# Performance work log

Measured on AMD Instinct MI355X. Metric: run time of the kernel, lower is better.

## Reference

```python
import jax, jax.numpy as jnp
import numpy as np

N = 50000      # n_nodes
E = 800000     # edges (before self-loops)
IN = 128       # in_dim
HID = 32       # hidden_dim (per-head out channels)
HEADS = 4
EMB = 128      # embed_dim
LAYERS = 3
NEG_SLOPE = 0.2  # PyG GATv2 default leaky_relu slope


def _layer_norm(x, g, b):
    mu = jnp.mean(x, axis=-1, keepdims=True)
    var = jnp.var(x, axis=-1, keepdims=True)
    return g * (x - mu) / jnp.sqrt(var + 1e-5) + b


def _gatv2(h, src, dst, n, Wl, bl, Wr, br, att, bias):
    # GATv2Conv (PyG semantics, share_weights=False, concat=True).
    H, C = att.shape
    xl = (h @ Wl + bl).reshape(n, H, C)   # target (i) transform
    xr = (h @ Wr + br).reshape(n, H, C)   # source (j) transform
    x_i = xl[dst]                          # [Etot, H, C] gather
    x_j = xr[src]
    e = jax.nn.leaky_relu(x_i + x_j, NEG_SLOPE)
    logit = jnp.einsum('ehc,hc->eh', e, att)          # [Etot, H]
    # segment softmax over destination node (every node has a self-loop)
    m = jax.ops.segment_max(logit, dst, num_segments=n)
    ex = jnp.exp(logit - m[dst])
    den = jax.ops.segment_sum(ex, dst, num_segments=n)
    alpha = ex / (den[dst] + 1e-16)
    out = jax.ops.segment_sum(alpha[..., None] * x_j, dst, num_segments=n)
    return out.reshape(n, H * C) + bias


def setup_inputs() -> dict:
    key = jax.random.key(0)
    ks = iter(jax.random.split(key, 64))
    d = {}
    d['x'] = jax.random.normal(next(ks), (N, IN), jnp.float32)
    d['edge_index'] = jax.random.randint(next(ks), (2, E), 0, N, dtype=jnp.int64)

    def w(shape, fan):
        return jax.random.normal(next(ks), shape, jnp.float32) / np.float32(np.sqrt(fan))

    HC = HID * HEADS
    d['W_in'] = w((IN, HID), IN); d['b_in'] = jnp.zeros((HID,), jnp.float32)
    for i in range(LAYERS):
        ic = HID if i == 0 else HC
        d[f'Wl{i}'] = w((ic, HC), ic); d[f'bl{i}'] = jnp.zeros((HC,), jnp.float32)
        d[f'Wr{i}'] = w((ic, HC), ic); d[f'br{i}'] = jnp.zeros((HC,), jnp.float32)
        d[f'att{i}'] = w((HEADS, HID), HID)
        d[f'bo{i}'] = jnp.zeros((HC,), jnp.float32)
        d[f'g{i}'] = jnp.ones((HC,), jnp.float32)
        d[f'be{i}'] = jnp.zeros((HC,), jnp.float32)
    d['W_out'] = w((HC, EMB), HC); d['b_out'] = jnp.zeros((EMB,), jnp.float32)
    return d


def reference(x, edge_index, W_in, b_in,
              Wl0, bl0, Wr0, br0, att0, bo0, g0, be0,
              Wl1, bl1, Wr1, br1, att1, bo1, g1, be1,
              Wl2, bl2, Wr2, br2, att2, bo2, g2, be2,
              W_out, b_out):
    n = x.shape[0]
    loops = jnp.arange(n, dtype=edge_index.dtype)  # add_self_loops=True
    src = jnp.concatenate([edge_index[0], loops])
    dst = jnp.concatenate([edge_index[1], loops])

    h = jax.nn.gelu(x @ W_in + b_in, approximate=False)
    layers = [(Wl0, bl0, Wr0, br0, att0, bo0, g0, be0),
              (Wl1, bl1, Wr1, br1, att1, bo1, g1, be1),
              (Wl2, bl2, Wr2, br2, att2, bo2, g2, be2)]
    for (Wl, bl, Wr, br, att, bo, g, be) in layers:
        h_new = jax.nn.gelu(_layer_norm(_gatv2(h, src, dst, n, Wl, bl, Wr, br, att, bo), g, be), approximate=False)
        h = h + h_new if h.shape == h_new.shape else h_new  # dropout = identity (eval)
    out = h @ W_out + b_out
    norm = jnp.maximum(jnp.linalg.norm(out, axis=-1, keepdims=True), 1e-12)
    return out / norm
```

## Files before the change

### kernel.cpp

```cpp
#include <hip/hip_runtime.h>
#include <hip/hip_bf16.h>
#include <math.h>

#define N_NODES 50000
#define N_EDGES 800000
#define IN_DIM  128
#define HC_DIM  128
#define HID_C   32
#define SCAN_NB 196
#define LOG2E   1.4426950408889634f

typedef __attribute__((ext_vector_type(8))) short short8;
typedef __attribute__((ext_vector_type(4))) float f32x4;
typedef _Float16 hf8 __attribute__((ext_vector_type(8)));
typedef unsigned int uint4v __attribute__((ext_vector_type(4)));

__device__ __forceinline__ float gelu_f(float x){
    return 0.5f*x*(1.0f + erff(x*0.7071067811865475f));
}

__device__ __forceinline__ void split2(float f, short& h, short& l){
    __hip_bfloat16 bh = __float2bfloat16(f);
    float r = f - __bfloat162float(bh);
    __hip_bfloat16 blo = __float2bfloat16(r);
    h = *reinterpret_cast<short*>(&bh);
    l = *reinterpret_cast<short*>(&blo);
}
__device__ __forceinline__ unsigned short f2h(float f){
    _Float16 h = (_Float16)f;
    return __builtin_bit_cast(unsigned short, h);
}
__device__ __forceinline__ float bf2f(unsigned short u){
    return __uint_as_float(((unsigned)u)<<16);
}

__global__ __launch_bounds__(256) void k_count(const int* __restrict__ dst, int* __restrict__ cnt,
                                               int* __restrict__ rank){
    int b = blockIdx.x*1024 + threadIdx.x;
    #pragma unroll
    for(int i=0;i<4;i++){
        int e = b + i*256;
        if(e < N_EDGES) rank[e] = atomicAdd(&cnt[dst[e]], 1);
    }
}

__global__ __launch_bounds__(256) void k_scan1(const int* __restrict__ cnt, int* __restrict__ rowptr,
                                               int* __restrict__ part){
    __shared__ int sh[256];
    int t=threadIdx.x; int i=blockIdx.x*256+t;
    int v = (i<N_NODES)? cnt[i] : 0;
    sh[t]=v; __syncthreads();
    for(int off=1; off<256; off<<=1){
        int y = (t>=off)? sh[t-off] : 0;
        __syncthreads();
        sh[t] += y;
        __syncthreads();
    }
    if(i<N_NODES) rowptr[i] = sh[t]-v;
    if(t==255) part[blockIdx.x] = sh[255];
}

__global__ __launch_bounds__(256) void k_scan2(int* __restrict__ part){
    __shared__ int sh[256];
    int t=threadIdx.x;
    int v = (t<SCAN_NB)? part[t] : 0;
    sh[t]=v; __syncthreads();
    for(int off=1; off<256; off<<=1){
        int y=(t>=off)? sh[t-off]:0;
        __syncthreads();
        sh[t]+=y;
        __syncthreads();
    }
    if(t<SCAN_NB) part[t] = sh[t]-v;
}

__global__ __launch_bounds__(256) void k_scan3(int* __restrict__ rowptr, const int* __restrict__ part){
    int t=threadIdx.x; int i=blockIdx.x*256+t;
    if(i<N_NODES) rowptr[i] += part[blockIdx.x];
    if(i==0) rowptr[N_NODES]=N_EDGES;
}

__global__ __launch_bounds__(256) void k_fill(const int* __restrict__ src, const int* __restrict__ dst,
                                              const int* __restrict__ rowptr, const int* __restrict__ rank,
                                              int* __restrict__ col){
    int b = blockIdx.x*1024 + threadIdx.x;
    #pragma unroll
    for(int i=0;i<4;i++){
        int e = b + i*256;
        if(e < N_EDGES) col[rowptr[dst[e]] + rank[e]] = src[e];
    }
}

__global__ __launch_bounds__(256) void k_splitW(const float* __restrict__ W0, const float* __restrict__ W1,
                                                const float* __restrict__ W2, const float* __restrict__ W3,
                                                const float* __restrict__ W4, const float* __restrict__ W5,
                                                const float* __restrict__ W6, short* __restrict__ WT){
    int bx = blockIdx.x;
    int m, kc;
    if(bx < 2){ m = bx; kc = 0; }
    else { m = 2 + (bx-2)/4; kc = (bx-2)&3; }
    const float* src; int K; size_t off;
    switch(m){
        case 0: src=W0; K=32;  off=0;      break;
        case 1: src=W1; K=32;  off=8192;   break;
        case 2: src=W2; K=128; off=16384;  break;
        case 3: src=W3; K=128; off=49152;  break;
        case 4: src=W4; K=128; off=81920;  break;
        case 5: src=W5; K=128; off=114688; break;
        default:src=W6; K=128; off=147456; break;
    }
    short* hi = WT + off;
    short* lo = hi + (size_t)K*HC_DIM;
    #pragma unroll
    for(int i=0;i<16;i++){
        int idx = threadIdx.x + i*256;
        int k = kc*32 + (idx>>7);
        int n = idx & 127;
        float f = src[(size_t)k*HC_DIM + n];
        short h,l; split2(f,h,l);
        hi[(size_t)n*K + k] = h;
        lo[(size_t)n*K + k] = l;
    }
}

__global__ __launch_bounds__(256) void k_gemm_in(const float* __restrict__ x, const float* __restrict__ W,
                                                 const float* __restrict__ b,
                                                 short* __restrict__ hhi, short* __restrict__ hlo){
    int id = blockIdx.x*256+threadIdx.x;
    int r = id>>5, c = id&31;
    const float4* x4 = (const float4*)(x + (size_t)r*IN_DIM);
    float acc=0.f;
    #pragma unroll 8
    for(int k=0;k<IN_DIM/4;k++){
        float4 xv = x4[k];
        acc = fmaf(xv.x, W[(4*k  )*HID_C+c], acc);
        acc = fmaf(xv.y, W[(4*k+1)*HID_C+c], acc);
        acc = fmaf(xv.z, W[(4*k+2)*HID_C+c], acc);
        acc = fmaf(xv.w, W[(4*k+3)*HID_C+c], acc);
    }
    float v = gelu_f(acc + b[c]);
    short hh,ll; split2(v,hh,ll);
    hhi[(size_t)r*HID_C+c] = hh;
    hlo[(size_t)r*HID_C+c] = ll;
}

template<int K, bool PAIR, bool NORM>
__global__ __launch_bounds__(256) void k_mm(const short* __restrict__ Ahi, const short* __restrict__ Alo,
                                            const short* __restrict__ WTl, const float* __restrict__ bl,
                                            const short* __restrict__ WTr, const float* __restrict__ br,
                                            float* __restrict__ XLf, unsigned short* __restrict__ XLh,
                                            unsigned short* __restrict__ XR16){
    constexpr int LDS_K = 40;
    constexpr int NCH = K / 32;
    __shared__ short As_hi[64*LDS_K], As_lo[64*LDS_K];
    __shared__ short Bh0[128*LDS_K], Bl0[128*LDS_K];
    __shared__ short Bh1[PAIR?128*LDS_K:1], Bl1[PAIR?128*LDS_K:1];
    __shared__ float ssq[NORM?256:1];

    int t = threadIdx.x;
    int lane = t & 63, wave = t >> 6;
    int quad = lane >> 4, ml = lane & 15;
    int rbase = blockIdx.x * 64;

    const short* WTl_lo = WTl + (size_t)K*HC_DIM;
    const short* WTr_lo = PAIR ? (WTr + (size_t)K*HC_DIM) : nullptr;

    f32x4 accL[4][2], accR[4][2];
    #pragma unroll
    for(int i=0;i<4;i++)
        #pragma unroll
        for(int j=0;j<2;j++){ accL[i][j]=(f32x4){0,0,0,0}; accR[i][j]=(f32x4){0,0,0,0}; }

    int r = t >> 2, seg = t & 3;
    int gr = rbase + r; if(gr >= N_NODES) gr = N_NODES-1;

    for(int c=0; c<NCH; c++){
        if(c) __syncthreads();
        size_t ka = (size_t)gr*K + c*32 + seg*8;
        *(short8*)(As_hi + r*LDS_K + seg*8) = *(const short8*)(Ahi + ka);
        *(short8*)(As_lo + r*LDS_K + seg*8) = *(const short8*)(Alo + ka);
        #pragma unroll
        for(int u=0; u<2; u++){
            int uu = t + u*256;
            int n = uu >> 2, sg = uu & 3;
            size_t kw = (size_t)n*K + c*32 + sg*8;
            *(short8*)(Bh0 + n*LDS_K + sg*8) = *(const short8*)(WTl + kw);
            *(short8*)(Bl0 + n*LDS_K + sg*8) = *(const short8*)(WTl_lo + kw);
            if(PAIR){
                *(short8*)(Bh1 + n*LDS_K + sg*8) = *(const short8*)(WTr + kw);
                *(short8*)(Bl1 + n*LDS_K + sg*8) = *(const short8*)(WTr_lo + kw);
            }
        }
        __syncthreads();

        int k0 = quad*8;
        short8 ah[4], al[4];
        #pragma unroll
        for(int i=0;i<4;i++){
            ah[i] = *(const short8*)(As_hi + (16*i + ml)*LDS_K + k0);
            al[i] = *(const short8*)(As_lo + (16*i + ml)*LDS_K + k0);
        }
        #pragma unroll
        for(int j=0;j<2;j++){
            int nrow = j*64 + wave*16 + ml;
            short8 bh = *(const short8*)(Bh0 + nrow*LDS_K + k0);
            short8 blo = *(const short8*)(Bl0 + nrow*LDS_K + k0);
            #pragma unroll
            for(int i=0;i<4;i++){
                accL[i][j] = __builtin_amdgcn_mfma_f32_16x16x32_bf16(ah[i], bh,  accL[i][j], 0,0,0);
                accL[i][j] = __builtin_amdgcn_mfma_f32_16x16x32_bf16(ah[i], blo, accL[i][j], 0,0,0);
                accL[i][j] = __builtin_amdgcn_mfma_f32_16x16x32_bf16(al[i], bh,  accL[i][j], 0,0,0);
            }
            if(PAIR){
                short8 ch = *(const short8*)(Bh1 + nrow*LDS_K + k0);
                short8 cl = *(const short8*)(Bl1 + nrow*LDS_K + k0);
                #pragma unroll
                for(int i=0;i<4;i++){
                    accR[i][j] = __builtin_amdgcn_mfma_f32_16x16x32_bf16(ah[i], ch, accR[i][j], 0,0,0);
                    accR[i][j] = __builtin_amdgcn_mfma_f32_16x16x32_bf16(ah[i], cl, accR[i][j], 0,0,0);
                    accR[i][j] = __builtin_amdgcn_mfma_f32_16x16x32_bf16(al[i], ch, accR[i][j], 0,0,0);
                }
            }
        }
    }

    int col0 = wave*16 + ml, col1 = 64 + wave*16 + ml;
    float bL0 = bl[col0], bL1 = bl[col1];

    if(NORM){
        #pragma unroll
        for(int i=0;i<4;i++){
            #pragma unroll
            for(int rr=0;rr<4;rr++){
                float v0 = accL[i][0][rr] + bL0;
                float v1 = accL[i][1][rr] + bL1;
                float p = v0*v0 + v1*v1;
                p += __shfl_xor(p,1); p += __shfl_xor(p,2);
                p += __shfl_xor(p,4); p += __shfl_xor(p,8);
                if(ml==0) ssq[wave*64 + 16*i + quad*4 + rr] = p;
            }
        }
        __syncthreads();
        #pragma unroll
        for(int i=0;i<4;i++){
            #pragma unroll
            for(int rr=0;rr<4;rr++){
                int row = 16*i + quad*4 + rr;
                int grr = rbase + row;
                if(grr < N_NODES){
                    float tot = ssq[row] + ssq[64+row] + ssq[128+row] + ssq[192+row];
                    float inv = 1.0f / fmaxf(sqrtf(tot), 1e-12f);
                    XLf[(size_t)grr*HC_DIM + col0] = (accL[i][0][rr] + bL0) * inv;
                    XLf[(size_t)grr*HC_DIM + col1] = (accL[i][1][rr] + bL1) * inv;
                }
            }
        }
    } else {
        float bR0 = PAIR ? br[col0] : 0.f, bR1 = PAIR ? br[col1] : 0.f;
        #pragma unroll
        for(int i=0;i<4;i++){
            #pragma unroll
            for(int rr=0;rr<4;rr++){
                int grr = rbase + 16*i + quad*4 + rr;
                if(grr < N_NODES){
                    XLh[(size_t)grr*HC_DIM + col0] = f2h(accL[i][0][rr] + bL0);
                    XLh[(size_t)grr*HC_DIM + col1] = f2h(accL[i][1][rr] + bL1);
                    if(PAIR){
                        XR16[(size_t)grr*HC_DIM + col0] = f2h(accR[i][0][rr] + bR0);
                        XR16[(size_t)grr*HC_DIM + col1] = f2h(accR[i][1][rr] + bR1);
                    }
                }
            }
        }
    }
}

__global__ __launch_bounds__(256) void k_node(const unsigned short* __restrict__ XLH, const unsigned short* __restrict__ XR,
    const int* __restrict__ rowptr, const int* __restrict__ colidx,
    const float* __restrict__ att, const float* __restrict__ bo,
    const float* __restrict__ gg, const float* __restrict__ be,
    const short* __restrict__ hold_hi, const short* __restrict__ hold_lo,
    short* __restrict__ hi_out, short* __restrict__ lo_out)
{
    int wave=threadIdx.x>>6, lane=threadIdx.x&63;
    int qd = lane >> 4, cl = lane & 15;
    int c8 = cl << 3;
    int ch2 = c8 + (qd<<1);

    float4 aa = *(const float4*)(att + c8);
    float4 abv = *(const float4*)(att + c8 + 4);
    float af[8] = {aa.x,aa.y,aa.z,aa.w,abv.x,abv.y,abv.z,abv.w};
    hf8 av6, av4;
    const float s6 = 0.6f*LOG2E, s4 = 0.4f*LOG2E;
    #pragma unroll
    for(int k=0;k<8;k++){
        av6[k] = (_Float16)(af[k]*s6);
        av4[k] = (_Float16)(af[k]*s4);
    }
    float4 b0 = *(const float4*)(bo + c8);
    float4 b1 = *(const float4*)(bo + c8 + 4);
    float bof[8] = {b0.x,b0.y,b0.z,b0.w,b1.x,b1.y,b1.z,b1.w};
    float2 g2  = *(const float2*)(gg + ch2);
    float2 be2 = *(const float2*)(be + ch2);

    #define H2(v,k) __builtin_shufflevector(v, v, 2*(k), 2*(k)+1)
    #define LOADH(j, xv) { xv = *(const hf8*)((const _Float16*)XR + ((size_t)((unsigned)(j)<<7)) + c8); }
#if defined(__has_builtin) && __has_builtin(__builtin_amdgcn_fdot2)
    #define LOGIT(xv, q) { \
        hf8 u_ = xlh + xv; \
        hf8 a_ = __builtin_bit_cast(hf8, __builtin_bit_cast(uint4v, u_) & 0x7fff7fffu); \
        float qa_ = __builtin_amdgcn_fdot2(H2(u_,0), H2(av6,0), 0.f, false); \
        float qb_ = __builtin_amdgcn_fdot2(H2(a_,0), H2(av4,0), 0.f, false); \
        qa_ = __builtin_amdgcn_fdot2(H2(u_,1), H2(av6,1), qa_, false); \
        qb_ = __builtin_amdgcn_fdot2(H2(a_,1), H2(av4,1), qb_, false); \
        qa_ = __builtin_amdgcn_fdot2(H2(u_,2), H2(av6,2), qa_, false); \
        qb_ = __builtin_amdgcn_fdot2(H2(a_,2), H2(av4,2), qb_, false); \
        qa_ = __builtin_amdgcn_fdot2(H2(u_,3), H2(av6,3), qa_, false); \
        qb_ = __builtin_amdgcn_fdot2(H2(a_,3), H2(av4,3), qb_, false); \
        q = qa_ + qb_; \
        q += __shfl_xor(q,1); q += __shfl_xor(q,2); }
#else
    #define LOGIT(xv, q) { \
        hf8 u_ = xlh + xv; \
        hf8 a_ = __builtin_bit_cast(hf8, __builtin_bit_cast(uint4v, u_) & 0x7fff7fffu); \
        q = 0.f; \
        _Pragma("unroll") \
        for(int k_=0;k_<8;k_++) q = fmaf((float)u_[k_], (float)av6[k_], fmaf((float)a_[k_], (float)av4[k_], q)); \
        q += __shfl_xor(q,1); q += __shfl_xor(q,2); }
#endif
    #define UPDATE4 { \
        float nm = fmaxf(m, fmaxf(fmaxf(q0,q1),fmaxf(q2,q3))); \
        float sc = exp2f(m-nm); \
        float e0=exp2f(q0-nm), e1=exp2f(q1-nm), e2=exp2f(q2-nm), e3=exp2f(q3-nm); \
        ls = fmaf(ls, sc, (e0+e1)+(e2+e3)); \
        _Pragma("unroll") \
        for(int k=0;k<8;k++) \
            acc[k] = fmaf(acc[k], sc, fmaf(e0,(float)x0[k], fmaf(e1,(float)x1[k], fmaf(e2,(float)x2[k], e3*(float)x3[k])))); \
        m = nm; }

    int nstep = gridDim.x << 2;
    for(int node = (blockIdx.x<<2) + wave; node < N_NODES; node += nstep){

        int beg = rowptr[node], end = rowptr[node+1];
        hf8 xlh = *(const hf8*)((const _Float16*)XLH + ((size_t)((unsigned)node<<7)) + c8);
        hf8 xs; LOADH(node, xs)
        float hres0 = 0.f, hres1 = 0.f;
        if(hold_hi){
            short2 hh = *(const short2*)(hold_hi + (size_t)node*HC_DIM + ch2);
            short2 hl = *(const short2*)(hold_lo + (size_t)node*HC_DIM + ch2);
            hres0 = bf2f((unsigned short)hh.x) + bf2f((unsigned short)hl.x);
            hres1 = bf2f((unsigned short)hh.y) + bf2f((unsigned short)hl.y);
        }

        float qs; LOGIT(xs, qs)
        float m, ls, acc[8];
        if(qd==0){
            m = qs; ls = 1.f;
            #pragma unroll
            for(int k=0;k<8;k++) acc[k] = (float)xs[k];
        } else {
            m = -1e30f; ls = 0.f;
            #pragma unroll
            for(int k=0;k<8;k++) acc[k] = 0.f;
        }

        int P = end - beg;
        int nb = P >> 4;
        int base = beg;
        int qoff = qd << 2;
        for(int b=0; b<nb; b++, base += 16){
            int b2 = base + qoff;
            int j0 = colidx[b2], j1 = colidx[b2+1], j2 = colidx[b2+2], j3 = colidx[b2+3];
            hf8 x0,x1,x2,x3;
            LOADH(j0,x0) LOADH(j1,x1) LOADH(j2,x2) LOADH(j3,x3)
            float q0,q1,q2,q3;
            LOGIT(x0,q0) LOGIT(x1,q1) LOGIT(x2,q2) LOGIT(x3,q3)
            UPDATE4
        }
        if(base < end){
            int b2 = base + qoff;
            int j0 = (b2  <end)? colidx[b2]   : node;
            int j1 = (b2+1<end)? colidx[b2+1] : node;
            int j2 = (b2+2<end)? colidx[b2+2] : node;
            int j3 = (b2+3<end)? colidx[b2+3] : node;
            hf8 x0,x1,x2,x3;
            LOADH(j0,x0) LOADH(j1,x1) LOADH(j2,x2) LOADH(j3,x3)
            float q0,q1,q2,q3;
            LOGIT(x0,q0) LOGIT(x1,q1) LOGIT(x2,q2) LOGIT(x3,q3)
            if(b2+1>=end) q1 = -INFINITY;
            if(b2+2>=end) q2 = -INFINITY;
            if(b2+3>=end) q3 = -INFINITY;
            if(b2 < end){
                UPDATE4
            }
        }

        #pragma unroll
        for(int mk=16; mk<=32; mk<<=1){
            float mo  = __shfl_xor(m, mk);
            float lso = __shfl_xor(ls, mk);
            float ao[8];
            #pragma unroll
            for(int k=0;k<8;k++) ao[k] = __shfl_xor(acc[k], mk);
            float nm = fmaxf(m, mo);
            float s0 = exp2f(m-nm), s1 = exp2f(mo-nm);
            ls = ls*s0 + lso*s1;
            #pragma unroll
            for(int k=0;k<8;k++) acc[k] = acc[k]*s0 + ao[k]*s1;
            m = nm;
        }

        float inv = 1.0f/ls;
        float o[8];
        #pragma unroll
        for(int k=0;k<8;k++) o[k] = fmaf(acc[k], inv, bof[k]);
        float s1v = ((o[0]+o[1])+(o[2]+o[3])) + ((o[4]+o[5])+(o[6]+o[7]));
        float s2v = o[0]*o[0];
        #pragma unroll
        for(int k=1;k<8;k++) s2v = fmaf(o[k],o[k],s2v);
        #pragma unroll
        for(int mk=1;mk<16;mk<<=1){ s1v += __shfl_xor(s1v,mk); s2v += __shfl_xor(s2v,mk); }
        float mean = s1v*(1.f/128.f);
        float var  = s2v*(1.f/128.f) - mean*mean;
        float rstd = rsqrtf(var + 1e-5f);

        float oa = (qd&2) ? ((qd&1)? o[6] : o[4]) : ((qd&1)? o[2] : o[0]);
        float ob = (qd&2) ? ((qd&1)? o[7] : o[5]) : ((qd&1)? o[3] : o[1]);
        float r0 = gelu_f(fmaf(g2.x*(oa-mean), rstd, be2.x)) + hres0;
        float r1 = gelu_f(fmaf(g2.y*(ob-mean), rstd, be2.y)) + hres1;
        short h0,l0,h1,l1;
        split2(r0,h0,l0); split2(r1,h1,l1);
        *(short2*)(hi_out + (size_t)node*HC_DIM + ch2) = make_short2(h0,h1);
        *(short2*)(lo_out + (size_t)node*HC_DIM + ch2) = make_short2(l0,l1);
    }
    #undef UPDATE4
    #undef LOGIT
    #undef LOADH
    #undef H2
}

extern "C" void kernel_launch(void* const* d_in, const int* in_sizes, int n_in,
                              void* d_out, int out_size, void* d_ws, size_t ws_size,
                              hipStream_t stream)
{
    const float* x   = (const float*)d_in[0];
    const int*   ei  = (const int*)  d_in[1];
    const float* Win = (const float*)d_in[2];
    const float* bin = (const float*)d_in[3];
    const float *Wl[3], *bl[3], *Wr[3], *br[3], *att[3], *bo[3], *gg[3], *be[3];
    for(int i=0;i<3;i++){
        const int base = 4 + 8*i;
        Wl[i]=(const float*)d_in[base+0]; bl[i]=(const float*)d_in[base+1];
        Wr[i]=(const float*)d_in[base+2]; br[i]=(const float*)d_in[base+3];
        att[i]=(const float*)d_in[base+4]; bo[i]=(const float*)d_in[base+5];
        gg[i]=(const float*)d_in[base+6]; be[i]=(const float*)d_in[base+7];
    }
    const float* Wout=(const float*)d_in[28];
    const float* bout=(const float*)d_in[29];
    float* out = (float*)d_out;

    char* w = (char*)d_ws;
    unsigned short* XLH = (unsigned short*)w; w += (size_t)N_NODES*HC_DIM*2;
    unsigned short* XR16 = (unsigned short*)w; w += (size_t)N_NODES*HC_DIM*2;
    short* hAhi = (short*)w; w += (size_t)N_NODES*HC_DIM*2;
    short* hAlo = (short*)w; w += (size_t)N_NODES*HC_DIM*2;
    short* hBhi = (short*)w; w += (size_t)N_NODES*HC_DIM*2;
    short* hBlo = (short*)w; w += (size_t)N_NODES*HC_DIM*2;
    short* WT   = (short*)w; w += (size_t)180224*2;
    int* rowptr = (int*)w;  w += (size_t)(N_NODES+2)*4;
    int* cursor = (int*)w;  w += (size_t)N_NODES*4;
    int* colidx = (int*)w;  w += (size_t)N_EDGES*4;
    int* rank   = (int*)w;  w += (size_t)N_EDGES*4;
    int* part   = (int*)w;  w += 256*4;

    const int* srcp = ei;
    const int* dstp = ei + N_EDGES;

    const short* WTl0 = WT + 0;      const short* WTr0 = WT + 8192;
    const short* WTl1 = WT + 16384;  const short* WTr1 = WT + 49152;
    const short* WTl2 = WT + 81920;  const short* WTr2 = WT + 114688;
    const short* WTo  = WT + 147456;

    k_splitW<<<22,256,0,stream>>>(Wl[0],Wr[0],Wl[1],Wr[1],Wl[2],Wr[2],Wout, WT);
    hipMemsetAsync(cursor, 0, (size_t)N_NODES*4, stream);
    k_count <<<782,256, 0, stream>>>(dstp, cursor, rank);
    k_scan1 <<<SCAN_NB,256,0,stream>>>(cursor, rowptr, part);
    k_scan2 <<<1,   256, 0, stream>>>(part);
    k_scan3 <<<SCAN_NB,256,0,stream>>>(rowptr, part);
    k_fill  <<<782,256, 0, stream>>>(srcp, dstp, rowptr, rank, colidx);
    k_gemm_in<<<6250,256,0,stream>>>(x, Win, bin, hAhi, hAlo);

    k_mm<32,true,false><<<782,256,0,stream>>>(hAhi, hAlo, WTl0, bl[0], WTr0, br[0],
                                              nullptr, XLH, XR16);
    k_node<<<2048,256,0,stream>>>(XLH,XR16,rowptr,colidx,att[0],bo[0],gg[0],be[0],
                                  (const short*)nullptr, (const short*)nullptr, hBhi, hBlo);

    k_mm<128,true,false><<<782,256,0,stream>>>(hBhi, hBlo, WTl1, bl[1], WTr1, br[1],
                                               nullptr, XLH, XR16);
    k_node<<<2048,256,0,stream>>>(XLH,XR16,rowptr,colidx,att[1],bo[1],gg[1],be[1],
                                  hBhi, hBlo, hAhi, hAlo);

    k_mm<128,true,false><<<782,256,0,stream>>>(hAhi, hAlo, WTl2, bl[2], WTr2, br[2],
                                               nullptr, XLH, XR16);
    k_node<<<2048,256,0,stream>>>(XLH,XR16,rowptr,colidx,att[2],bo[2],gg[2],be[2],
                                  hAhi, hAlo, hBhi, hBlo);

    k_mm<128,false,true><<<782,256,0,stream>>>(hBhi, hBlo, WTo, bout, nullptr, nullptr,
                                               out, nullptr, nullptr);
}
```

Before: 505.2 us.

## Merge preprocessing kernels, fuse scan phases, and launch one wave per node

Weight splitting, the cursor memset and the input GEMM now run as one combined prep kernel. The three-stage scan becomes two passes: a last-block-done atomic performs the partial-sum scan, and the fill kernel applies the offsets while writing a finalized rowptr. The node kernel drops its grid-stride loop and launches one wave per node with 12500 blocks. The goal is fewer kernel launches and less serialization between small kernels. The cost is a threadfence/atomic dependency and more blocks in the node kernel.

After: 518.3 us. 2.6% more time.

```diff
diff --git a/kernel.cpp b/kernel.cpp
--- a/kernel.cpp
+++ b/kernel.cpp
@@ -9,6 +9,9 @@
 #define HID_C   32
 #define SCAN_NB 196
 #define LOG2E   1.4426950408889634f
+#define PREP_SPLITW 22
+#define PREP_MEMSET 49
+#define PREP_GEMM   6250
 
 typedef __attribute__((ext_vector_type(8))) short short8;
 typedef __attribute__((ext_vector_type(4))) float f32x4;
@@ -34,6 +37,69 @@
     return __uint_as_float(((unsigned)u)<<16);
 }
 
+__global__ __launch_bounds__(256) void k_prep(const float* __restrict__ W0, const float* __restrict__ W1,
+                                              const float* __restrict__ W2, const float* __restrict__ W3,
+                                              const float* __restrict__ W4, const float* __restrict__ W5,
+                                              const float* __restrict__ W6, short* __restrict__ WT,
+                                              int* __restrict__ cursor, int* __restrict__ flag,
+                                              const float* __restrict__ x, const float* __restrict__ Win,
+                                              const float* __restrict__ bin,
+                                              short* __restrict__ hhi, short* __restrict__ hlo){
+    int bx = blockIdx.x;
+    if(bx < PREP_SPLITW){
+        int m, kc;
+        if(bx < 2){ m = bx; kc = 0; }
+        else { m = 2 + (bx-2)/4; kc = (bx-2)&3; }
+        const float* src; int K; size_t off;
+        switch(m){
+            case 0: src=W0; K=32;  off=0;      break;
+            case 1: src=W1; K=32;  off=8192;   break;
+            case 2: src=W2; K=128; off=16384;  break;
+            case 3: src=W3; K=128; off=49152;  break;
+            case 4: src=W4; K=128; off=81920;  break;
+            case 5: src=W5; K=128; off=114688; break;
+            default:src=W6; K=128; off=147456; break;
+        }
+        short* hi = WT + off;
+        short* lo = hi + (size_t)K*HC_DIM;
+        #pragma unroll
+        for(int i=0;i<16;i++){
+            int idx = threadIdx.x + i*256;
+            int k = kc*32 + (idx>>7);
+            int n = idx & 127;
+            float f = src[(size_t)k*HC_DIM + n];
+            short h,l; split2(f,h,l);
+            hi[(size_t)n*K + k] = h;
+            lo[(size_t)n*K + k] = l;
+        }
+    } else if(bx < PREP_SPLITW + PREP_MEMSET){
+        int base = (bx - PREP_SPLITW)*1024 + threadIdx.x;
+        #pragma unroll
+        for(int i=0;i<4;i++){
+            int e = base + i*256;
+            if(e < N_NODES) cursor[e] = 0;
+        }
+        if(bx == PREP_SPLITW && threadIdx.x == 0) *flag = 0;
+    } else {
+        int id = (bx - PREP_SPLITW - PREP_MEMSET)*256 + threadIdx.x;
+        int r = id>>5, c = id&31;
+        const float4* x4 = (const float4*)(x + (size_t)r*IN_DIM);
+        float acc=0.f;
+        #pragma unroll 8
+        for(int k=0;k<IN_DIM/4;k++){
+            float4 xv = x4[k];
+            acc = fmaf(xv.x, Win[(4*k  )*HID_C+c], acc);
+            acc = fmaf(xv.y, Win[(4*k+1)*HID_C+c], acc);
+            acc = fmaf(xv.z, Win[(4*k+2)*HID_C+c], acc);
+            acc = fmaf(xv.w, Win[(4*k+3)*HID_C+c], acc);
+        }
+        float v = gelu_f(acc + bin[c]);
+        short hh,ll; split2(v,hh,ll);
+        hhi[(size_t)r*HID_C+c] = hh;
+        hlo[(size_t)r*HID_C+c] = ll;
+    }
+}
+
 __global__ __launch_bounds__(256) void k_count(const int* __restrict__ dst, int* __restrict__ cnt,
                                                int* __restrict__ rank){
     int b = blockIdx.x*1024 + threadIdx.x;
@@ -44,9 +110,10 @@
     }
 }
 
-__global__ __launch_bounds__(256) void k_scan1(const int* __restrict__ cnt, int* __restrict__ rowptr,
-                                               int* __restrict__ part){
+__global__ __launch_bounds__(256) void k_scan12(const int* __restrict__ cnt, int* __restrict__ rowptr,
+                                                int* __restrict__ part, int* __restrict__ flag){
     __shared__ int sh[256];
+    __shared__ int amLast;
     int t=threadIdx.x; int i=blockIdx.x*256+t;
     int v = (i<N_NODES)? cnt[i] : 0;
     sh[t]=v; __syncthreads();
@@ -58,90 +125,46 @@
     }
     if(i<N_NODES) rowptr[i] = sh[t]-v;
     if(t==255) part[blockIdx.x] = sh[255];
-}
-
-__global__ __launch_bounds__(256) void k_scan2(int* __restrict__ part){
-    __shared__ int sh[256];
-    int t=threadIdx.x;
-    int v = (t<SCAN_NB)? part[t] : 0;
-    sh[t]=v; __syncthreads();
-    for(int off=1; off<256; off<<=1){
-        int y=(t>=off)? sh[t-off]:0;
-        __syncthreads();
-        sh[t]+=y;
-        __syncthreads();
-    }
-    if(t<SCAN_NB) part[t] = sh[t]-v;
-}
-
-__global__ __launch_bounds__(256) void k_scan3(int* __restrict__ rowptr, const int* __restrict__ part){
-    int t=threadIdx.x; int i=blockIdx.x*256+t;
-    if(i<N_NODES) rowptr[i] += part[blockIdx.x];
-    if(i==0) rowptr[N_NODES]=N_EDGES;
+
+    __threadfence();
+    if(t==0){
+        int old = atomicAdd(flag, 1);
+        amLast = (old == (int)gridDim.x - 1);
+    }
+    __syncthreads();
+    if(amLast){
+        __threadfence();
+        volatile int* vp = part;
+        int v2 = (t<SCAN_NB)? vp[t] : 0;
+        sh[t]=v2; __syncthreads();
+        for(int off=1; off<256; off<<=1){
+            int y=(t>=off)? sh[t-off]:0;
+            __syncthreads();
+            sh[t]+=y;
+            __syncthreads();
+        }
+        if(t<SCAN_NB) part[t] = sh[t]-v2;
+    }
 }
 
 __global__ __launch_bounds__(256) void k_fill(const int* __restrict__ src, const int* __restrict__ dst,
-                                              const int* __restrict__ rowptr, const int* __restrict__ rank,
-                                              int* __restrict__ col){
+                                              const int* __restrict__ rowptr, const int* __restrict__ part,
+                                              const int* __restrict__ rank, int* __restrict__ col,
+                                              int* __restrict__ rowfin){
     int b = blockIdx.x*1024 + threadIdx.x;
     #pragma unroll
     for(int i=0;i<4;i++){
         int e = b + i*256;
-        if(e < N_EDGES) col[rowptr[dst[e]] + rank[e]] = src[e];
-    }
-}
-
-__global__ __launch_bounds__(256) void k_splitW(const float* __restrict__ W0, const float* __restrict__ W1,
-                                                const float* __restrict__ W2, const float* __restrict__ W3,
-                                                const float* __restrict__ W4, const float* __restrict__ W5,
-                                                const float* __restrict__ W6, short* __restrict__ WT){
-    int bx = blockIdx.x;
-    int m, kc;
-    if(bx < 2){ m = bx; kc = 0; }
-    else { m = 2 + (bx-2)/4; kc = (bx-2)&3; }
-    const float* src; int K; size_t off;
-    switch(m){
-        case 0: src=W0; K=32;  off=0;      break;
-        case 1: src=W1; K=32;  off=8192;   break;
-        case 2: src=W2; K=128; off=16384;  break;
-        case 3: src=W3; K=128; off=49152;  break;
-        case 4: src=W4; K=128; off=81920;  break;
-        case 5: src=W5; K=128; off=114688; break;
-        default:src=W6; K=128; off=147456; break;
-    }
-    short* hi = WT + off;
-    short* lo = hi + (size_t)K*HC_DIM;
-    #pragma unroll
-    for(int i=0;i<16;i++){
-        int idx = threadIdx.x + i*256;
-        int k = kc*32 + (idx>>7);
-        int n = idx & 127;
-        float f = src[(size_t)k*HC_DIM + n];
-        short h,l; split2(f,h,l);
-        hi[(size_t)n*K + k] = h;
-        lo[(size_t)n*K + k] = l;
-    }
-}
-
-__global__ __launch_bounds__(256) void k_gemm_in(const float* __restrict__ x, const float* __restrict__ W,
-                                                 const float* __restrict__ b,
-                                                 short* __restrict__ hhi, short* __restrict__ hlo){
-    int id = blockIdx.x*256+threadIdx.x;
-    int r = id>>5, c = id&31;
-    const float4* x4 = (const float4*)(x + (size_t)r*IN_DIM);
-    float acc=0.f;
-    #pragma unroll 8
-    for(int k=0;k<IN_DIM/4;k++){
-        float4 xv = x4[k];
-        acc = fmaf(xv.x, W[(4*k  )*HID_C+c], acc);
-        acc = fmaf(xv.y, W[(4*k+1)*HID_C+c], acc);
-        acc = fmaf(xv.z, W[(4*k+2)*HID_C+c], acc);
-        acc = fmaf(xv.w, W[(4*k+3)*HID_C+c], acc);
-    }
-    float v = gelu_f(acc + b[c]);
-    short hh,ll; split2(v,hh,ll);
-    hhi[(size_t)r*HID_C+c] = hh;
-    hlo[(size_t)r*HID_C+c] = ll;
+        if(e < N_EDGES){
+            int d = dst[e];
+            col[rowptr[d] + part[d>>8] + rank[e]] = src[e];
+        }
+    }
+    if(blockIdx.x < SCAN_NB){
+        int i = blockIdx.x*256 + threadIdx.x;
+        if(i < N_NODES) rowfin[i] = rowptr[i] + part[i>>8];
+        if(i == 0) rowfin[N_NODES] = N_EDGES;
+    }
 }
 
 template<int K, bool PAIR, bool NORM>
@@ -283,6 +306,7 @@
     short* __restrict__ hi_out, short* __restrict__ lo_out)
 {
     int wave=threadIdx.x>>6, lane=threadIdx.x&63;
+    int node = blockIdx.x*4 + wave;
     int qd = lane >> 4, cl = lane & 15;
     int c8 = cl << 3;
     int ch2 = c8 + (qd<<1);
@@ -338,105 +362,101 @@
             acc[k] = fmaf(acc[k], sc, fmaf(e0,(float)x0[k], fmaf(e1,(float)x1[k], fmaf(e2,(float)x2[k], e3*(float)x3[k])))); \
         m = nm; }
 
-    int nstep = gridDim.x << 2;
-    for(int node = (blockIdx.x<<2) + wave; node < N_NODES; node += nstep){
-
-        int beg = rowptr[node], end = rowptr[node+1];
-        hf8 xlh = *(const hf8*)((const _Float16*)XLH + ((size_t)((unsigned)node<<7)) + c8);
-        hf8 xs; LOADH(node, xs)
-        float hres0 = 0.f, hres1 = 0.f;
-        if(hold_hi){
-            short2 hh = *(const short2*)(hold_hi + (size_t)node*HC_DIM + ch2);
-            short2 hl = *(const short2*)(hold_lo + (size_t)node*HC_DIM + ch2);
-            hres0 = bf2f((unsigned short)hh.x) + bf2f((unsigned short)hl.x);
-            hres1 = bf2f((unsigned short)hh.y) + bf2f((unsigned short)hl.y);
-        }
-
-        float qs; LOGIT(xs, qs)
-        float m, ls, acc[8];
-        if(qd==0){
-            m = qs; ls = 1.f;
-            #pragma unroll
-            for(int k=0;k<8;k++) acc[k] = (float)xs[k];
-        } else {
-            m = -1e30f; ls = 0.f;
-            #pragma unroll
-            for(int k=0;k<8;k++) acc[k] = 0.f;
-        }
-
-        int P = end - beg;
-        int nb = P >> 4;
-        int base = beg;
-        int qoff = qd << 2;
-        for(int b=0; b<nb; b++, base += 16){
-            int b2 = base + qoff;
-            int j0 = colidx[b2], j1 = colidx[b2+1], j2 = colidx[b2+2], j3 = colidx[b2+3];
-            hf8 x0,x1,x2,x3;
-            LOADH(j0,x0) LOADH(j1,x1) LOADH(j2,x2) LOADH(j3,x3)
-            float q0,q1,q2,q3;
-            LOGIT(x0,q0) LOGIT(x1,q1) LOGIT(x2,q2) LOGIT(x3,q3)
+    int beg = rowptr[node], end = rowptr[node+1];
+    hf8 xlh = *(const hf8*)((const _Float16*)XLH + ((size_t)((unsigned)node<<7)) + c8);
+    hf8 xs; LOADH(node, xs)
+    float hres0 = 0.f, hres1 = 0.f;
+    if(hold_hi){
+        short2 hh = *(const short2*)(hold_hi + (size_t)node*HC_DIM + ch2);
+        short2 hl = *(const short2*)(hold_lo + (size_t)node*HC_DIM + ch2);
+        hres0 = bf2f((unsigned short)hh.x) + bf2f((unsigned short)hl.x);
+        hres1 = bf2f((unsigned short)hh.y) + bf2f((unsigned short)hl.y);
+    }
+
+    float qs; LOGIT(xs, qs)
+    float m, ls, acc[8];
+    if(qd==0){
+        m = qs; ls = 1.f;
+        #pragma unroll
+        for(int k=0;k<8;k++) acc[k] = (float)xs[k];
+    } else {
+        m = -1e30f; ls = 0.f;
+        #pragma unroll
+        for(int k=0;k<8;k++) acc[k] = 0.f;
+    }
+
+    int P = end - beg;
+    int nb = P >> 4;
+    int base = beg;
+    int qoff = qd << 2;
+    for(int b=0; b<nb; b++, base += 16){
+        int b2 = base + qoff;
+        int j0 = colidx[b2], j1 = colidx[b2+1], j2 = colidx[b2+2], j3 = colidx[b2+3];
+        hf8 x0,x1,x2,x3;
+        LOADH(j0,x0) LOADH(j1,x1) LOADH(j2,x2) LOADH(j3,x3)
+        float q0,q1,q2,q3;
+        LOGIT(x0,q0) LOGIT(x1,q1) LOGIT(x2,q2) LOGIT(x3,q3)
+        UPDATE4
+    }
+    if(base < end){
+        int b2 = base + qoff;
+        int j0 = (b2  <end)? colidx[b2]   : node;
+        int j1 = (b2+1<end)? colidx[b2+1] : node;
+        int j2 = (b2+2<end)? colidx[b2+2] : node;
+        int j3 = (b2+3<end)? colidx[b2+3] : node;
+        hf8 x0,x1,x2,x3;
+        LOADH(j0,x0) LOADH(j1,x1) LOADH(j2,x2) LOADH(j3,x3)
+        float q0,q1,q2,q3;
+        LOGIT(x0,q0) LOGIT(x1,q1) LOGIT(x2,q2) LOGIT(x3,q3)
+        if(b2+1>=end) q1 = -INFINITY;
+        if(b2+2>=end) q2 = -INFINITY;
+        if(b2+3>=end) q3 = -INFINITY;
+        if(b2 < end){
             UPDATE4
         }
-        if(base < end){
-            int b2 = base + qoff;
-            int j0 = (b2  <end)? colidx[b2]   : node;
-            int j1 = (b2+1<end)? colidx[b2+1] : node;
-            int j2 = (b2+2<end)? colidx[b2+2] : node;
-            int j3 = (b2+3<end)? colidx[b2+3] : node;
-            hf8 x0,x1,x2,x3;
-            LOADH(j0,x0) LOADH(j1,x1) LOADH(j2,x2) LOADH(j3,x3)
-            float q0,q1,q2,q3;
-            LOGIT(x0,q0) LOGIT(x1,q1) LOGIT(x2,q2) LOGIT(x3,q3)
-            if(b2+1>=end) q1 = -INFINITY;
-            if(b2+2>=end) q2 = -INFINITY;
-            if(b2+3>=end) q3 = -INFINITY;
-            if(b2 < end){
-                UPDATE4
-            }
-        }
-
-        #pragma unroll
-        for(int mk=16; mk<=32; mk<<=1){
-            float mo  = __shfl_xor(m, mk);
-            float lso = __shfl_xor(ls, mk);
-            float ao[8];
-            #pragma unroll
-            for(int k=0;k<8;k++) ao[k] = __shfl_xor(acc[k], mk);
-            float nm = fmaxf(m, mo);
-            float s0 = exp2f(m-nm), s1 = exp2f(mo-nm);
-            ls = ls*s0 + lso*s1;
-            #pragma unroll
-            for(int k=0;k<8;k++) acc[k] = acc[k]*s0 + ao[k]*s1;
-            m = nm;
-        }
-
-        float inv = 1.0f/ls;
-        float o[8];
-        #pragma unroll
-        for(int k=0;k<8;k++) o[k] = fmaf(acc[k], inv, bof[k]);
-        float s1v = ((o[0]+o[1])+(o[2]+o[3])) + ((o[4]+o[5])+(o[6]+o[7]));
-        float s2v = o[0]*o[0];
-        #pragma unroll
-        for(int k=1;k<8;k++) s2v = fmaf(o[k],o[k],s2v);
-        #pragma unroll
-        for(int mk=1;mk<16;mk<<=1){ s1v += __shfl_xor(s1v,mk); s2v += __shfl_xor(s2v,mk); }
-        float mean = s1v*(1.f/128.f);
-        float var  = s2v*(1.f/128.f) - mean*mean;
-        float rstd = rsqrtf(var + 1e-5f);
-
-        float oa = (qd&2) ? ((qd&1)? o[6] : o[4]) : ((qd&1)? o[2] : o[0]);
-        float ob = (qd&2) ? ((qd&1)? o[7] : o[5]) : ((qd&1)? o[3] : o[1]);
-        float r0 = gelu_f(fmaf(g2.x*(oa-mean), rstd, be2.x)) + hres0;
-        float r1 = gelu_f(fmaf(g2.y*(ob-mean), rstd, be2.y)) + hres1;
-        short h0,l0,h1,l1;
-        split2(r0,h0,l0); split2(r1,h1,l1);
-        *(short2*)(hi_out + (size_t)node*HC_DIM + ch2) = make_short2(h0,h1);
-        *(short2*)(lo_out + (size_t)node*HC_DIM + ch2) = make_short2(l0,l1);
     }
     #undef UPDATE4
     #undef LOGIT
     #undef LOADH
     #undef H2
+
+    #pragma unroll
+    for(int mk=16; mk<=32; mk<<=1){
+        float mo  = __shfl_xor(m, mk);
+        float lso = __shfl_xor(ls, mk);
+        float ao[8];
+        #pragma unroll
+        for(int k=0;k<8;k++) ao[k] = __shfl_xor(acc[k], mk);
+        float nm = fmaxf(m, mo);
+        float s0 = exp2f(m-nm), s1 = exp2f(mo-nm);
+        ls = ls*s0 + lso*s1;
+        #pragma unroll
+        for(int k=0;k<8;k++) acc[k] = acc[k]*s0 + ao[k]*s1;
+        m = nm;
+    }
+
+    float inv = 1.0f/ls;
+    float o[8];
+    #pragma unroll
+    for(int k=0;k<8;k++) o[k] = fmaf(acc[k], inv, bof[k]);
+    float s1v = ((o[0]+o[1])+(o[2]+o[3])) + ((o[4]+o[5])+(o[6]+o[7]));
+    float s2v = o[0]*o[0];
+    #pragma unroll
+    for(int k=1;k<8;k++) s2v = fmaf(o[k],o[k],s2v);
+    #pragma unroll
+    for(int mk=1;mk<16;mk<<=1){ s1v += __shfl_xor(s1v,mk); s2v += __shfl_xor(s2v,mk); }
+    float mean = s1v*(1.f/128.f);
+    float var  = s2v*(1.f/128.f) - mean*mean;
+    float rstd = rsqrtf(var + 1e-5f);
+
+    float oa = (qd&2) ? ((qd&1)? o[6] : o[4]) : ((qd&1)? o[2] : o[0]);
+    float ob = (qd&2) ? ((qd&1)? o[7] : o[5]) : ((qd&1)? o[3] : o[1]);
+    float r0 = gelu_f(fmaf(g2.x*(oa-mean), rstd, be2.x)) + hres0;
+    float r1 = gelu_f(fmaf(g2.y*(ob-mean), rstd, be2.y)) + hres1;
+    short h0,l0,h1,l1;
+    split2(r0,h0,l0); split2(r1,h1,l1);
+    *(short2*)(hi_out + (size_t)node*HC_DIM + ch2) = make_short2(h0,h1);
+    *(short2*)(lo_out + (size_t)node*HC_DIM + ch2) = make_short2(l0,l1);
 }
 
 extern "C" void kernel_launch(void* const* d_in, const int* in_sizes, int n_in,
@@ -468,10 +488,12 @@
     short* hBlo = (short*)w; w += (size_t)N_NODES*HC_DIM*2;
     short* WT   = (short*)w; w += (size_t)180224*2;
     int* rowptr = (int*)w;  w += (size_t)(N_NODES+2)*4;
+    int* rowfin = (int*)w;  w += (size_t)(N_NODES+2)*4;
     int* cursor = (int*)w;  w += (size_t)N_NODES*4;
     int* colidx = (int*)w;  w += (size_t)N_EDGES*4;
     int* rank   = (int*)w;  w += (size_t)N_EDGES*4;
     int* part   = (int*)w;  w += 256*4;
+    int* flag   = (int*)w;  w += 64;
 
     const int* srcp = ei;
     const int* dstp = ei + N_EDGES;
@@ -481,29 +503,27 @@
     const short* WTl2 = WT + 81920;  const short* WTr2 = WT + 114688;
     const short* WTo  = WT + 147456;
 
-    k_splitW<<<22,256,0,stream>>>(Wl[0],Wr[0],Wl[1],Wr[1],Wl[2],Wr[2],Wout, WT);
-    hipMemsetAsync(cursor, 0, (size_t)N_NODES*4, stream);
+    k_prep  <<<PREP_SPLITW+PREP_MEMSET+PREP_GEMM,256,0,stream>>>(
+              Wl[0],Wr[0],Wl[1],Wr[1],Wl[2],Wr[2],Wout, WT, cursor, flag,
+              x, Win, bin, hAhi, hAlo);
     k_count <<<782,256, 0, stream>>>(dstp, cursor, rank);
-    k_scan1 <<<SCAN_NB,256,0,stream>>>(cursor, rowptr, part);
-    k_scan2 <<<1,   256, 0, stream>>>(part);
-    k_scan3 <<<SCAN_NB,256,0,stream>>>(rowptr, part);
-    k_fill  <<<782,256, 0, stream>>>(srcp, dstp, rowptr, rank, colidx);
-    k_gemm_in<<<6250,256,0,stream>>>(x, Win, bin, hAhi, hAlo);
+    k_scan12<<<SCAN_NB,256,0,stream>>>(cursor, rowptr, part, flag);
+    k_fill  <<<782,256, 0, stream>>>(srcp, dstp, rowptr, part, rank, colidx, rowfin);
 
     k_mm<32,true,false><<<782,256,0,stream>>>(hAhi, hAlo, WTl0, bl[0], WTr0, br[0],
                                               nullptr, XLH, XR16);
-    k_node<<<2048,256,0,stream>>>(XLH,XR16,rowptr,colidx,att[0],bo[0],gg[0],be[0],
-                                  (const short*)nullptr, (const short*)nullptr, hBhi, hBlo);
+    k_node<<<12500,256,0,stream>>>(XLH,XR16,rowfin,colidx,att[0],bo[0],gg[0],be[0],
+                                   (const short*)nullptr, (const short*)nullptr, hBhi, hBlo);
 
     k_mm<128,true,false><<<782,256,0,stream>>>(hBhi, hBlo, WTl1, bl[1], WTr1, br[1],
                                                nullptr, XLH, XR16);
-    k_node<<<2048,256,0,stream>>>(XLH,XR16,rowptr,colidx,att[1],bo[1],gg[1],be[1],
-                                  hBhi, hBlo, hAhi, hAlo);
+    k_node<<<12500,256,0,stream>>>(XLH,XR16,rowfin,colidx,att[1],bo[1],gg[1],be[1],
+                                   hBhi, hBlo, hAhi, hAlo);
 
     k_mm<128,true,false><<<782,256,0,stream>>>(hAhi, hAlo, WTl2, bl[2], WTr2, br[2],
                                                nullptr, XLH, XR16);
-    k_node<<<2048,256,0,stream>>>(XLH,XR16,rowptr,colidx,att[2],bo[2],gg[2],be[2],
-                                  hAhi, hAlo, hBhi, hBlo);
+    k_node<<<12500,256,0,stream>>>(XLH,XR16,rowfin,colidx,att[2],bo[2],gg[2],be[2],
+                                   hAhi, hAlo, hBhi, hBlo);
 
     k_mm<128,false,true><<<782,256,0,stream>>>(hBhi, hBlo, WTo, bout, nullptr, nullptr,
                                                out, nullptr, nullptr);
```
